# Kernel optimization log

Hardware: AMD Instinct MI355X
Metric: run time of the kernel (lower is better)

Reference implementation:

```python
import jax, jax.numpy as jnp
import numpy as np

# AdaMem / network constants hardcoded in the torch module (mode='FULL')
BETA = 0.99        # membrane decay
THR_INIT = 1.0     # initial threshold (reset_mem)
SCALE = 5.0        # threshold adaptation jump per spike
THR_DECAY = 0.95   # threshold decay toward base
BASE_THR = 0.0     # base threshold
T = 200            # timesteps
B = 32             # batch
N_IN = 100 * 100   # fc1 input features
N_OUT = 3          # fc1 output features


def setup_inputs() -> dict:
    key = jax.random.key(0)
    k1, k2, k3, k4 = jax.random.split(key, 4)
    # sgen.rate: Bernoulli spikes with per-pixel probability = pixel intensity,
    # sampled independently at each of T timesteps -> [T, B, N_IN] in {0,1}
    intensity = jax.random.uniform(k1, (B, N_IN))
    spikes = (jax.random.uniform(k2, (T, B, N_IN)) < intensity).astype(jnp.float32)
    # fc1 parameters (Linear(10000, 3))
    W = jax.random.normal(k3, (N_OUT, N_IN), dtype=jnp.float32) * 0.01
    b = jax.random.normal(k4, (N_OUT,), dtype=jnp.float32) * 0.01
    return {"spikes": spikes, "W": W, "b": b}


def reference(spikes, W, b):
    # Batch all 200 independent linear projections into one GEMM: [T,B,N_IN] x [N_OUT,N_IN]
    proj = jnp.einsum('tbi,oi->tbo', spikes, W) + b  # [T, B, 3]

    def step(carry, x_t):
        mem, thr = carry
        mem = BETA * mem + x_t                       # leaky integration
        spk = (mem > thr).astype(mem.dtype)          # fire
        mem = mem - spk * thr                        # reset by subtraction
        thr = BASE_THR + THR_DECAY * (thr - BASE_THR) + SCALE * spk  # adaptive threshold
        return (mem, thr), (spk, mem)

    mem0 = jnp.zeros((B, N_OUT), dtype=proj.dtype)
    thr0 = jnp.full((B, N_OUT), THR_INIT, dtype=proj.dtype)
    _, (spk_rec, mem_rec) = jax.lax.scan(step, (mem0, thr0), proj)
    return spk_rec, mem_rec  # each [T, B, 3]
```

## Files before the change

### kernel.cpp

```cpp
#include <hip/hip_runtime.h>

#define T_STEPS 200
#define BATCH 32
#define N_IN 10000
#define N_OUT 3
#define ROWS (T_STEPS * BATCH)
#define PROJ_N (T_STEPS * BATCH * N_OUT)

__global__ __launch_bounds__(256) void proj_kernel(
    const float* __restrict__ spikes,
    const float* __restrict__ W,
    float* __restrict__ proj)
{
    const int row = blockIdx.x;
    const int tid = threadIdx.x;

    const float4* __restrict__ srow = reinterpret_cast<const float4*>(spikes + (size_t)row * N_IN);
    const float4* __restrict__ W0 = reinterpret_cast<const float4*>(W);
    const float4* __restrict__ W1 = reinterpret_cast<const float4*>(W + N_IN);
    const float4* __restrict__ W2 = reinterpret_cast<const float4*>(W + 2 * N_IN);

    float a0 = 0.f, a1 = 0.f, a2 = 0.f;
    #pragma unroll 2
    for (int i = tid; i < N_IN / 4; i += 256) {
        float4 s  = srow[i];
        float4 w0 = W0[i];
        float4 w1 = W1[i];
        float4 w2 = W2[i];
        a0 += s.x * w0.x + s.y * w0.y + s.z * w0.z + s.w * w0.w;
        a1 += s.x * w1.x + s.y * w1.y + s.z * w1.z + s.w * w1.w;
        a2 += s.x * w2.x + s.y * w2.y + s.z * w2.z + s.w * w2.w;
    }

    for (int off = 32; off > 0; off >>= 1) {
        a0 += __shfl_down(a0, off);
        a1 += __shfl_down(a1, off);
        a2 += __shfl_down(a2, off);
    }

    __shared__ float red0[4], red1[4], red2[4];
    const int wave = tid >> 6;
    if ((tid & 63) == 0) { red0[wave] = a0; red1[wave] = a1; red2[wave] = a2; }
    __syncthreads();
    if (tid == 0) {
        float r0 = red0[0] + red0[1] + red0[2] + red0[3];
        float r1 = red1[0] + red1[1] + red1[2] + red1[3];
        float r2 = red2[0] + red2[1] + red2[2] + red2[3];
        proj[row * 3 + 0] = r0;
        proj[row * 3 + 1] = r1;
        proj[row * 3 + 2] = r2;
    }
}

__global__ __launch_bounds__(128) void scan_kernel(
    const float* __restrict__ bias,
    float* __restrict__ out)
{
    const int idx = threadIdx.x;
    if (idx >= BATCH * N_OUT) return;

    const float bo = bias[idx % N_OUT];
    float* __restrict__ spk_rec = out;
    float* __restrict__ mem_rec = out + PROJ_N;

    float mem = 0.0f;
    float thr = 1.0f;

    for (int t = 0; t < T_STEPS; ++t) {
        const int e = t * (BATCH * N_OUT) + idx;
        float x = spk_rec[e] + bo;
        mem = 0.99f * mem + x;
        float spk = (mem > thr) ? 1.0f : 0.0f;
        mem = mem - spk * thr;
        thr = 0.95f * thr + 5.0f * spk;
        spk_rec[e] = spk;
        mem_rec[e] = mem;
    }
}

extern "C" void kernel_launch(void* const* d_in, const int* in_sizes, int n_in,
                              void* d_out, int out_size, void* d_ws, size_t ws_size,
                              hipStream_t stream) {
    const float* spikes = (const float*)d_in[0];
    const float* W      = (const float*)d_in[1];
    const float* b      = (const float*)d_in[2];
    float* out = (float*)d_out;

    proj_kernel<<<ROWS, 256, 0, stream>>>(spikes, W, out );
    scan_kernel<<<1, 128, 0, stream>>>(b, out);
}
```

Measured before the change: 62.26 us.

## Process four rows per block to reuse W loads and batch scan input loads

The projection kernel now handles four spike rows per block, so each loaded W vector is reused across four rows and the block count drops by four. Bias is added inside the projection, and results go to a workspace buffer instead of the output buffer. The scan kernel prefetches eight timesteps of inputs at a time, so its serial loop waits on memory less often. Fewer blocks means less parallelism and more registers per thread. The main cost, streaming the spikes tensor, is unchanged.

```diff
diff --git a/kernel.cpp b/kernel.cpp
--- a/kernel.cpp
+++ b/kernel.cpp
@@ -5,76 +5,101 @@
 #define N_IN 10000
 #define N_OUT 3
 #define ROWS (T_STEPS * BATCH)
-#define PROJ_N (T_STEPS * BATCH * N_OUT)
+#define STATES (BATCH * N_OUT)
+#define PROJ_N (ROWS * N_OUT)
+#define NV4 (N_IN / 4)
+#define RPB 4
+
+__device__ __forceinline__ float dot4(float4 a, float4 b) {
+    return a.x * b.x + a.y * b.y + a.z * b.z + a.w * b.w;
+}
 
 __global__ __launch_bounds__(256) void proj_kernel(
     const float* __restrict__ spikes,
     const float* __restrict__ W,
+    const float* __restrict__ bias,
     float* __restrict__ proj)
 {
-    const int row = blockIdx.x;
+    const int row0 = blockIdx.x * RPB;
     const int tid = threadIdx.x;
 
-    const float4* __restrict__ srow = reinterpret_cast<const float4*>(spikes + (size_t)row * N_IN);
+    const float4* __restrict__ s0 = reinterpret_cast<const float4*>(spikes + (size_t)row0 * N_IN);
     const float4* __restrict__ W0 = reinterpret_cast<const float4*>(W);
     const float4* __restrict__ W1 = reinterpret_cast<const float4*>(W + N_IN);
     const float4* __restrict__ W2 = reinterpret_cast<const float4*>(W + 2 * N_IN);
 
-    float a0 = 0.f, a1 = 0.f, a2 = 0.f;
+    float acc[RPB][3];
+    #pragma unroll
+    for (int r = 0; r < RPB; ++r)
+        #pragma unroll
+        for (int o = 0; o < 3; ++o) acc[r][o] = 0.f;
+
     #pragma unroll 2
-    for (int i = tid; i < N_IN / 4; i += 256) {
-        float4 s  = srow[i];
+    for (int i = tid; i < NV4; i += 256) {
         float4 w0 = W0[i];
         float4 w1 = W1[i];
         float4 w2 = W2[i];
-        a0 += s.x * w0.x + s.y * w0.y + s.z * w0.z + s.w * w0.w;
-        a1 += s.x * w1.x + s.y * w1.y + s.z * w1.z + s.w * w1.w;
-        a2 += s.x * w2.x + s.y * w2.y + s.z * w2.z + s.w * w2.w;
+        #pragma unroll
+        for (int r = 0; r < RPB; ++r) {
+            float4 s = s0[(size_t)r * NV4 + i];
+            acc[r][0] += dot4(s, w0);
+            acc[r][1] += dot4(s, w1);
+            acc[r][2] += dot4(s, w2);
+        }
     }
 
-    for (int off = 32; off > 0; off >>= 1) {
-        a0 += __shfl_down(a0, off);
-        a1 += __shfl_down(a1, off);
-        a2 += __shfl_down(a2, off);
+    #pragma unroll
+    for (int r = 0; r < RPB; ++r)
+        #pragma unroll
+        for (int o = 0; o < 3; ++o)
+            for (int off = 32; off > 0; off >>= 1)
+                acc[r][o] += __shfl_down(acc[r][o], off);
+
+    __shared__ float red[4][RPB][3];
+    const int wave = tid >> 6;
+    if ((tid & 63) == 0) {
+        #pragma unroll
+        for (int r = 0; r < RPB; ++r)
+            #pragma unroll
+            for (int o = 0; o < 3; ++o)
+                red[wave][r][o] = acc[r][o];
     }
-
-    __shared__ float red0[4], red1[4], red2[4];
-    const int wave = tid >> 6;
-    if ((tid & 63) == 0) { red0[wave] = a0; red1[wave] = a1; red2[wave] = a2; }
     __syncthreads();
-    if (tid == 0) {
-        float r0 = red0[0] + red0[1] + red0[2] + red0[3];
-        float r1 = red1[0] + red1[1] + red1[2] + red1[3];
-        float r2 = red2[0] + red2[1] + red2[2] + red2[3];
-        proj[row * 3 + 0] = r0;
-        proj[row * 3 + 1] = r1;
-        proj[row * 3 + 2] = r2;
+    if (tid < RPB * 3) {
+        const int r = tid / 3, o = tid % 3;
+        float s = red[0][r][o] + red[1][r][o] + red[2][r][o] + red[3][r][o];
+        proj[(size_t)(row0 + r) * 3 + o] = s + bias[o];
     }
 }
 
 __global__ __launch_bounds__(128) void scan_kernel(
-    const float* __restrict__ bias,
+    const float* __restrict__ proj,
     float* __restrict__ out)
 {
     const int idx = threadIdx.x;
-    if (idx >= BATCH * N_OUT) return;
+    if (idx >= STATES) return;
 
-    const float bo = bias[idx % N_OUT];
     float* __restrict__ spk_rec = out;
     float* __restrict__ mem_rec = out + PROJ_N;
 
     float mem = 0.0f;
     float thr = 1.0f;
 
-    for (int t = 0; t < T_STEPS; ++t) {
-        const int e = t * (BATCH * N_OUT) + idx;
-        float x = spk_rec[e] + bo;
-        mem = 0.99f * mem + x;
-        float spk = (mem > thr) ? 1.0f : 0.0f;
-        mem = mem - spk * thr;
-        thr = 0.95f * thr + 5.0f * spk;
-        spk_rec[e] = spk;
-        mem_rec[e] = mem;
+    float xb[8];
+    for (int t0 = 0; t0 < T_STEPS; t0 += 8) {
+        #pragma unroll
+        for (int k = 0; k < 8; ++k)
+            xb[k] = proj[(size_t)(t0 + k) * STATES + idx];
+        #pragma unroll
+        for (int k = 0; k < 8; ++k) {
+            mem = 0.99f * mem + xb[k];
+            float spk = (mem > thr) ? 1.0f : 0.0f;
+            mem -= spk * thr;
+            thr = 0.95f * thr + 5.0f * spk;
+            const int e = (t0 + k) * STATES + idx;
+            spk_rec[e] = spk;
+            mem_rec[e] = mem;
+        }
     }
 }
 
@@ -84,8 +109,9 @@
     const float* spikes = (const float*)d_in[0];
     const float* W      = (const float*)d_in[1];
     const float* b      = (const float*)d_in[2];
-    float* out = (float*)d_out;
+    float* out  = (float*)d_out;
+    float* proj = (float*)d_ws;
 
-    proj_kernel<<<ROWS, 256, 0, stream>>>(spikes, W, out );
-    scan_kernel<<<1, 128, 0, stream>>>(b, out);
+    proj_kernel<<<ROWS / RPB, 256, 0, stream>>>(spikes, W, b, proj);
+    scan_kernel<<<1, 128, 0, stream>>>(proj, out);
 }
```

Result: faster. 55.62 us (-10.7%).
